# Kernel optimization log

Measured on AMD Instinct MI355X. Metric: run time of the kernel, lower is better.

## Reference

```python
import jax, jax.numpy as jnp
import numpy as np

B, S, H, NH = 8, 1024, 1024, 4
D = H // NH
NEG = jnp.float32(-2**32 + 1)


def setup_inputs() -> dict:
    key = jax.random.key(0)
    ks = jax.random.split(key, 12)
    w = 1.0 / np.sqrt(H)
    wf = 1.0 / np.sqrt(2 * H)
    return {
        "memory": jax.random.normal(ks[0], (B, S, H), jnp.float32),
        "decoder_input": jax.random.normal(ks[1], (B, S, H), jnp.float32),
        "mask": jax.random.bernoulli(ks[2], 0.2, (B, S, S)),
        "query_mask": (jax.random.uniform(ks[3], (B, S)) > 0.1).astype(jnp.float32),
        "Wk": jax.random.normal(ks[4], (H, H), jnp.float32) * w,
        "Wv": jax.random.normal(ks[5], (H, H), jnp.float32) * w,
        "Wq": jax.random.normal(ks[6], (H, H), jnp.float32) * w,
        "Wf": jax.random.normal(ks[7], (2 * H, H), jnp.float32) * wf,
        "bf": jnp.zeros((H,), jnp.float32),
        "gamma": jnp.ones((H,), jnp.float32),
        "beta": jnp.zeros((H,), jnp.float32),
        "g_factor": jax.random.uniform(ks[8], (1,), jnp.float32, 1e4, 2e4),
    }


def reference(memory, decoder_input, mask, query_mask, Wk, Wv, Wq, Wf, bf, gamma, beta, g_factor):
    b, sq, hdim = decoder_input.shape
    sk = memory.shape[1]

    def heads(x, W, s):  # -> (NH, B, s, D), matching torch permute(2,0,1,3)
        return (x @ W).reshape(b, s, NH, D).transpose(2, 0, 1, 3)

    k = heads(memory, Wk, sk)
    v = heads(memory, Wv, sk)
    q = heads(decoder_input, Wq, sq)

    attn = jnp.einsum("hbqd,hbkd->hbqk", q, k) / jnp.sqrt(jnp.float32(D))
    idx = jnp.arange(sk, dtype=jnp.float32)
    gauss = (idx[:, None] - idx[None, :]) ** 2 / g_factor[0]  # (sq, sk), sq==sk
    attn = attn - gauss
    attn = jnp.where(mask[None], NEG, attn)
    attn = jax.nn.softmax(attn, axis=-1)
    attn = attn * query_mask[None, :, :, None]  # post-softmax query mask

    res = jnp.einsum("hbqk,hbkd->hbqd", attn, v)
    res = res.transpose(1, 2, 0, 3).reshape(b, sq, hdim)

    out = jnp.concatenate([decoder_input, res], axis=-1) @ Wf + bf
    out = out + decoder_input
    mu = out.mean(-1, keepdims=True)
    var = ((out - mu) ** 2).mean(-1, keepdims=True)
    out = (out - mu) / jnp.sqrt(var + 1e-5) * gamma + beta
    return out, attn.reshape(NH * b, sq, sk)
```

## Files before the change

kernel.cpp:

```cpp
#include <hip/hip_runtime.h>

#define B_ 8
#define S_ 1024
#define H_ 1024
#define NH_ 4
#define D_ 256
#define M_ 8192

typedef unsigned int u32;
typedef unsigned short u16;
typedef __attribute__((ext_vector_type(4))) float f32x4;
typedef __attribute__((ext_vector_type(8))) short s16x8;

__device__ __forceinline__ float bf2f(u16 b) { return __uint_as_float(((u32)b) << 16); }
__device__ __forceinline__ u16 f2bf(float f) {
    u32 x = __float_as_uint(f);
    return (u16)((x + 0x7fffu + ((x >> 16) & 1u)) >> 16);
}

__global__ void init_flags_k(int* fl) { fl[0] = 0; fl[1] = 0; fl[2] = 0; }

__global__ __launch_bounds__(256) void or_mask_k(const u32* __restrict__ m, int* __restrict__ fl) {
    u32 v = m[blockIdx.x * 256 + threadIdx.x];
#pragma unroll
    for (int o = 32; o; o >>= 1) v |= __shfl_xor(v, o, 64);
    if ((threadIdx.x & 63) == 0) atomicOr(fl + 1, (int)v);
}

__global__ void classify_mask_k(int* fl) {
    u32 R = (u32)fl[1];
    int c;
    if (R == 0x3F803F80u)      c = 2;
    else if (R == 0x3F800000u) c = 3;
    else if (R & 0xFFFFFF00u)  c = 0;
    else                       c = 1;
    fl[2] = c;
}

__global__ __launch_bounds__(256) void tcast_k(const float* __restrict__ src, u16* __restrict__ dst,
                                               int R, int C) {
    __shared__ float sb[32][33];
    const int c0 = blockIdx.x * 32, r0 = blockIdx.y * 32;
    const int tx = threadIdx.x & 31, ty = threadIdx.x >> 5;
#pragma unroll
    for (int i = 0; i < 4; i++)
        sb[ty + 8 * i][tx] = src[(size_t)(r0 + ty + 8 * i) * C + c0 + tx];
    __syncthreads();
#pragma unroll
    for (int i = 0; i < 4; i++)
        dst[(size_t)(c0 + ty + 8 * i) * R + r0 + tx] = f2bf(sb[tx][ty + 8 * i]);
}

template<int AMODE>
__device__ __forceinline__ void gemm_core(
    const float* __restrict__ A32, const u16* __restrict__ A16, int lda,
    const u16* __restrict__ Bp, int ldb, int K, int m0, int n0,
    short* As, short* Bs, f32x4 acc[4][4])
{
    const int t = threadIdx.x;
    const int lane = t & 63, wave = t >> 6;
    const int wy = wave >> 1, wx = wave & 1;
    const int mq = lane >> 4, ml = lane & 15;
    const int srow = t >> 2, skq = t & 3;

    for (int k0 = 0; k0 < K; k0 += 32) {
        __syncthreads();
#pragma unroll
        for (int it = 0; it < 2; it++) {
            const int row = srow + it * 64;
            const int kk = k0 + skq * 8;
            short* dst = As + row * 40 + skq * 8;
            if (AMODE == 0) {
                const float* s = A32 + (size_t)(m0 + row) * lda + kk;
                float4 v0 = *(const float4*)s, v1 = *(const float4*)(s + 4);
                s16x8 p;
                p[0] = (short)f2bf(v0.x); p[1] = (short)f2bf(v0.y);
                p[2] = (short)f2bf(v0.z); p[3] = (short)f2bf(v0.w);
                p[4] = (short)f2bf(v1.x); p[5] = (short)f2bf(v1.y);
                p[6] = (short)f2bf(v1.z); p[7] = (short)f2bf(v1.w);
                *(s16x8*)dst = p;
            } else if (AMODE == 1) {
                *(s16x8*)dst = *(const s16x8*)(A16 + (size_t)(m0 + row) * lda + kk);
            } else {
                if (kk < 1024) {
                    const float* s = A32 + (size_t)(m0 + row) * 1024 + kk;
                    float4 v0 = *(const float4*)s, v1 = *(const float4*)(s + 4);
                    s16x8 p;
                    p[0] = (short)f2bf(v0.x); p[1] = (short)f2bf(v0.y);
                    p[2] = (short)f2bf(v0.z); p[3] = (short)f2bf(v0.w);
                    p[4] = (short)f2bf(v1.x); p[5] = (short)f2bf(v1.y);
                    p[6] = (short)f2bf(v1.z); p[7] = (short)f2bf(v1.w);
                    *(s16x8*)dst = p;
                } else {
                    *(s16x8*)dst = *(const s16x8*)(A16 + (size_t)(m0 + row) * 1024 + (kk - 1024));
                }
            }
        }
#pragma unroll
        for (int it = 0; it < 2; it++) {
            const int row = srow + it * 64;
            *(s16x8*)(Bs + row * 40 + skq * 8) =
                *(const s16x8*)(Bp + (size_t)(n0 + row) * ldb + k0 + skq * 8);
        }
        __syncthreads();
        s16x8 af[4], bfr[4];
#pragma unroll
        for (int i = 0; i < 4; i++) {
            af[i]  = *(s16x8*)(As + (wy * 64 + i * 16 + ml) * 40 + mq * 8);
            bfr[i] = *(s16x8*)(Bs + (wx * 64 + i * 16 + ml) * 40 + mq * 8);
        }
#pragma unroll
        for (int mi = 0; mi < 4; mi++)
#pragma unroll
            for (int ni = 0; ni < 4; ni++)
                acc[mi][ni] = __builtin_amdgcn_mfma_f32_16x16x32_bf16(af[mi], bfr[ni], acc[mi][ni], 0, 0, 0);
    }
}

__global__ __launch_bounds__(256) void gemm_proj_k(const float* __restrict__ A, const u16* __restrict__ WT,
                                                   u16* __restrict__ C) {
    __shared__ short As[128 * 40];
    __shared__ short Bs[128 * 40];
    const int m0 = blockIdx.y * 128, n0 = blockIdx.x * 128;
    f32x4 acc[4][4];
#pragma unroll
    for (int i = 0; i < 4; i++)
#pragma unroll
        for (int j = 0; j < 4; j++) acc[i][j] = 0;
    gemm_core<0>(A, nullptr, H_, WT, H_, H_, m0, n0, As, Bs, acc);
    const int lane = threadIdx.x & 63, wave = threadIdx.x >> 6;
    const int wy = wave >> 1, wx = wave & 1, mq = lane >> 4, ml = lane & 15;
#pragma unroll
    for (int mi = 0; mi < 4; mi++)
#pragma unroll
        for (int ni = 0; ni < 4; ni++) {
            const int n = n0 + wx * 64 + ni * 16 + ml;
#pragma unroll
            for (int r = 0; r < 4; r++) {
                const int m = m0 + wy * 64 + mi * 16 + mq * 4 + r;
                C[(size_t)m * H_ + n] = f2bf(acc[mi][ni][r]);
            }
        }
}

__global__ __launch_bounds__(256) void gemm_vt_k(const float* __restrict__ A, const u16* __restrict__ WT,
                                                 u16* __restrict__ VT) {
    __shared__ short As[128 * 40];
    __shared__ short Bs[128 * 40];
    const int m0 = blockIdx.y * 128, n0 = blockIdx.x * 128;
    f32x4 acc[4][4];
#pragma unroll
    for (int i = 0; i < 4; i++)
#pragma unroll
        for (int j = 0; j < 4; j++) acc[i][j] = 0;
    gemm_core<0>(A, nullptr, H_, WT, H_, H_, m0, n0, As, Bs, acc);
    const int lane = threadIdx.x & 63, wave = threadIdx.x >> 6;
    const int wy = wave >> 1, wx = wave & 1, mq = lane >> 4, ml = lane & 15;
#pragma unroll
    for (int mi = 0; mi < 4; mi++)
#pragma unroll
        for (int ni = 0; ni < 4; ni++) {
            const int n = n0 + wx * 64 + ni * 16 + ml;
            const int mbase = m0 + wy * 64 + mi * 16 + mq * 4;
            const int b = mbase >> 10, s = mbase & 1023;
            ushort4 w;
            w.x = f2bf(acc[mi][ni][0]); w.y = f2bf(acc[mi][ni][1]);
            w.z = f2bf(acc[mi][ni][2]); w.w = f2bf(acc[mi][ni][3]);
            *(ushort4*)(VT + ((size_t)(b * 1024 + n)) * 1024 + s) = w;
        }
}

__global__ __launch_bounds__(256) void qk_logits_k(const u16* __restrict__ Qb, const u16* __restrict__ Kb,
                                                   const void* __restrict__ mask,
                                                   const float* __restrict__ gfac, const int* __restrict__ fl,
                                                   float* __restrict__ logits) {
    __shared__ short As[128 * 40];
    __shared__ short Bs[128 * 40];
    const int z = blockIdx.z, h = z >> 3, b = z & 7;
    const u16* Aq = Qb + (size_t)b * S_ * H_ + h * D_;
    const u16* Bk = Kb + (size_t)b * S_ * H_ + h * D_;
    const int m0 = blockIdx.y * 128, n0 = blockIdx.x * 128;
    f32x4 acc[4][4];
#pragma unroll
    for (int i = 0; i < 4; i++)
#pragma unroll
        for (int j = 0; j < 4; j++) acc[i][j] = 0;
    gemm_core<1>(nullptr, Aq, H_, Bk, H_, D_, m0, n0, As, Bs, acc);
    const float g = gfac[0];
    const int code = fl[2];
    const int lane = threadIdx.x & 63, wave = threadIdx.x >> 6;
    const int wy = wave >> 1, wx = wave & 1, mq = lane >> 4, ml = lane & 15;
#pragma unroll
    for (int mi = 0; mi < 4; mi++)
#pragma unroll
        for (int ni = 0; ni < 4; ni++) {
            const int kg = n0 + wx * 64 + ni * 16 + ml;
#pragma unroll
            for (int r = 0; r < 4; r++) {
                const int qg = m0 + wy * 64 + mi * 16 + mq * 4 + r;
                float diff = (float)(qg - kg);
                float val = acc[mi][ni][r] * 0.0625f - diff * diff / g;
                size_t midx = ((size_t)b * S_ + qg) * S_ + kg;
                int mv;
                if (code == 0)      mv = ((const unsigned char*)mask)[midx];
                else if (code == 1) mv = ((const int*)mask)[midx];
                else if (code == 2) mv = (((const u16*)mask)[midx] != 0);
                else                mv = (((const u32*)mask)[midx] != 0);
                if (mv) val = -4294967296.0f;
                logits[((size_t)z * S_ + qg) * S_ + kg] = val;
            }
        }
}

__global__ __launch_bounds__(256) void softmax_k(float* __restrict__ logits, const float* __restrict__ qmask) {
    const int row = blockIdx.x;
    const int b = (row >> 10) & 7, qg = row & 1023;
    float* p = logits + (size_t)row * S_;
    const int t = threadIdx.x, wave = t >> 6;
    float4 v = ((const float4*)p)[t];
    __shared__ float red[4];
    float mx = fmaxf(fmaxf(v.x, v.y), fmaxf(v.z, v.w));
#pragma unroll
    for (int o = 32; o; o >>= 1) mx = fmaxf(mx, __shfl_xor(mx, o, 64));
    if ((t & 63) == 0) red[wave] = mx;
    __syncthreads();
    mx = fmaxf(fmaxf(red[0], red[1]), fmaxf(red[2], red[3]));
    __syncthreads();
    v.x = __expf(v.x - mx); v.y = __expf(v.y - mx);
    v.z = __expf(v.z - mx); v.w = __expf(v.w - mx);
    float s = v.x + v.y + v.z + v.w;
#pragma unroll
    for (int o = 32; o; o >>= 1) s += __shfl_xor(s, o, 64);
    if ((t & 63) == 0) red[wave] = s;
    __syncthreads();
    s = red[0] + red[1] + red[2] + red[3];
    const float sc = qmask[b * S_ + qg] / s;
    v.x *= sc; v.y *= sc; v.z *= sc; v.w *= sc;
    ((float4*)p)[t] = v;
}

__global__ __launch_bounds__(256) void pv_mfma_k(const float* __restrict__ attnF, const u16* __restrict__ VT,
                                                 u16* __restrict__ resB) {
    __shared__ short As[128 * 40];
    __shared__ short Bs[128 * 40];
    const int z = blockIdx.z, h = z >> 3, b = z & 7;
    const float* Ap = attnF + (size_t)z * S_ * S_;
    const u16* Bp = VT + ((size_t)(b * 1024 + h * D_)) * 1024;
    const int m0 = blockIdx.y * 128, n0 = blockIdx.x * 128;
    f32x4 acc[4][4];
#pragma unroll
    for (int i = 0; i < 4; i++)
#pragma unroll
        for (int j = 0; j < 4; j++) acc[i][j] = 0;
    gemm_core<0>(Ap, nullptr, S_, Bp, 1024, S_, m0, n0, As, Bs, acc);
    u16* C = resB + (size_t)b * S_ * H_ + h * D_;
    const int lane = threadIdx.x & 63, wave = threadIdx.x >> 6;
    const int wy = wave >> 1, wx = wave & 1, mq = lane >> 4, ml = lane & 15;
#pragma unroll
    for (int mi = 0; mi < 4; mi++)
#pragma unroll
        for (int ni = 0; ni < 4; ni++) {
            const int n = n0 + wx * 64 + ni * 16 + ml;
#pragma unroll
            for (int r = 0; r < 4; r++) {
                const int m = m0 + wy * 64 + mi * 16 + mq * 4 + r;
                C[(size_t)m * H_ + n] = f2bf(acc[mi][ni][r]);
            }
        }
}

__global__ __launch_bounds__(256) void final_mfma_k(const float* __restrict__ dec, const u16* __restrict__ resB,
                                                    const u16* __restrict__ WfT, const float* __restrict__ bfv,
                                                    u16* __restrict__ tmp) {
    __shared__ short As[128 * 40];
    __shared__ short Bs[128 * 40];
    const int m0 = blockIdx.y * 128, n0 = blockIdx.x * 128;
    f32x4 acc[4][4];
#pragma unroll
    for (int i = 0; i < 4; i++)
#pragma unroll
        for (int j = 0; j < 4; j++) acc[i][j] = 0;
    gemm_core<2>(dec, resB, H_, WfT, 2048, 2048, m0, n0, As, Bs, acc);
    const int lane = threadIdx.x & 63, wave = threadIdx.x >> 6;
    const int wy = wave >> 1, wx = wave & 1, mq = lane >> 4, ml = lane & 15;
#pragma unroll
    for (int mi = 0; mi < 4; mi++)
#pragma unroll
        for (int ni = 0; ni < 4; ni++) {
            const int n = n0 + wx * 64 + ni * 16 + ml;
#pragma unroll
            for (int r = 0; r < 4; r++) {
                const int m = m0 + wy * 64 + mi * 16 + mq * 4 + r;
                float val = acc[mi][ni][r] + bfv[n] + dec[(size_t)m * H_ + n];
                tmp[(size_t)m * H_ + n] = f2bf(val);
            }
        }
}

__global__ __launch_bounds__(256) void ln2_k(const u16* __restrict__ tmp, const float* __restrict__ gm,
                                             const float* __restrict__ bt, float* __restrict__ out) {
    const int m = blockIdx.x, t = threadIdx.x;
    ushort4 u = ((const ushort4*)(tmp + (size_t)m * H_))[t];
    float xa[4] = {bf2f(u.x), bf2f(u.y), bf2f(u.z), bf2f(u.w)};
    float s = 0.f, s2 = 0.f;
#pragma unroll
    for (int i = 0; i < 4; i++) { s += xa[i]; s2 += xa[i] * xa[i]; }
#pragma unroll
    for (int o = 32; o; o >>= 1) { s += __shfl_xor(s, o, 64); s2 += __shfl_xor(s2, o, 64); }
    __shared__ float rs[4], rs2[4];
    if ((t & 63) == 0) { rs[t >> 6] = s; rs2[t >> 6] = s2; }
    __syncthreads();
    s  = rs[0] + rs[1] + rs[2] + rs[3];
    s2 = rs2[0] + rs2[1] + rs2[2] + rs2[3];
    float mu = s * (1.f / 1024.f);
    float var = s2 * (1.f / 1024.f) - mu * mu;
    float rstd = rsqrtf(var + 1e-5f);
    float ov[4];
#pragma unroll
    for (int i = 0; i < 4; i++) {
        int n = t * 4 + i;
        ov[i] = (xa[i] - mu) * rstd * gm[n] + bt[n];
    }
    *(float4*)(out + (size_t)m * H_ + t * 4) = make_float4(ov[0], ov[1], ov[2], ov[3]);
}

extern "C" void kernel_launch(void* const* d_in, const int* in_sizes, int n_in,
                              void* d_out, int out_size, void* d_ws, size_t ws_size,
                              hipStream_t stream) {
    const float* memory = (const float*)d_in[0];
    const float* dec    = (const float*)d_in[1];
    const void*  mask   = d_in[2];
    const float* qmask  = (const float*)d_in[3];
    const float* Wk     = (const float*)d_in[4];
    const float* Wv     = (const float*)d_in[5];
    const float* Wq     = (const float*)d_in[6];
    const float* Wf     = (const float*)d_in[7];
    const float* bfv    = (const float*)d_in[8];
    const float* gamma  = (const float*)d_in[9];
    const float* beta   = (const float*)d_in[10];
    const float* gfac   = (const float*)d_in[11];

    char* ws = (char*)d_ws;
    int* fl  = (int*)ws;
    u16* WqT = (u16*)(ws + (1u  << 20));
    u16* WkT = (u16*)(ws + (3u  << 20));
    u16* WvT = (u16*)(ws + (5u  << 20));
    u16* WfT = (u16*)(ws + (7u  << 20));
    u16* Qb  = (u16*)(ws + (11u << 20));
    u16* Kb  = (u16*)(ws + (27u << 20));
    u16* VT  = (u16*)(ws + (43u << 20));
    u16* resB = Kb;
    u16* tmpB = Qb;

    float* out   = (float*)d_out;
    float* attnF = out + (size_t)B_ * S_ * H_;

    init_flags_k<<<1, 1, 0, stream>>>(fl);
    or_mask_k<<<256, 256, 0, stream>>>((const u32*)mask, fl);
    classify_mask_k<<<1, 1, 0, stream>>>(fl);

    tcast_k<<<dim3(32, 32), 256, 0, stream>>>(Wq, WqT, 1024, 1024);
    tcast_k<<<dim3(32, 32), 256, 0, stream>>>(Wk, WkT, 1024, 1024);
    tcast_k<<<dim3(32, 32), 256, 0, stream>>>(Wv, WvT, 1024, 1024);
    tcast_k<<<dim3(32, 64), 256, 0, stream>>>(Wf, WfT, 2048, 1024);

    gemm_proj_k<<<dim3(8, 64), 256, 0, stream>>>(dec,    WqT, Qb);
    gemm_proj_k<<<dim3(8, 64), 256, 0, stream>>>(memory, WkT, Kb);
    gemm_vt_k  <<<dim3(8, 64), 256, 0, stream>>>(memory, WvT, VT);

    qk_logits_k<<<dim3(8, 8, 32), 256, 0, stream>>>(Qb, Kb, mask, gfac, fl, attnF);
    softmax_k<<<32768, 256, 0, stream>>>(attnF, qmask);
    pv_mfma_k<<<dim3(2, 8, 32), 256, 0, stream>>>(attnF, VT, resB);
    final_mfma_k<<<dim3(8, 64), 256, 0, stream>>>(dec, resB, WfT, bfv, tmpB);
    ln2_k<<<M_, 256, 0, stream>>>(tmpB, gamma, beta, out);
}
```

Measured before the change: 696.1 us.

## Fuse QK logits with row softmax and pre-cast projection inputs to bf16

```diff
diff --git a/kernel.cpp b/kernel.cpp
--- a/kernel.cpp
+++ b/kernel.cpp
@@ -49,6 +49,14 @@
 #pragma unroll
     for (int i = 0; i < 4; i++)
         dst[(size_t)(c0 + ty + 8 * i) * R + r0 + tx] = f2bf(sb[tx][ty + 8 * i]);
+}
+
+__global__ __launch_bounds__(256) void castbf_k(const float* __restrict__ src, u16* __restrict__ dst) {
+    const int i = blockIdx.x * 256 + threadIdx.x;
+    float4 v = ((const float4*)src)[i];
+    ushort4 o;
+    o.x = f2bf(v.x); o.y = f2bf(v.y); o.z = f2bf(v.z); o.w = f2bf(v.w);
+    ((ushort4*)dst)[i] = o;
 }
 
 template<int AMODE>
@@ -117,7 +125,7 @@
     }
 }
 
-__global__ __launch_bounds__(256) void gemm_proj_k(const float* __restrict__ A, const u16* __restrict__ WT,
+__global__ __launch_bounds__(256) void gemm_proj_k(const u16* __restrict__ A, const u16* __restrict__ WT,
                                                    u16* __restrict__ C) {
     __shared__ short As[128 * 40];
     __shared__ short Bs[128 * 40];
@@ -127,7 +135,7 @@
     for (int i = 0; i < 4; i++)
 #pragma unroll
         for (int j = 0; j < 4; j++) acc[i][j] = 0;
-    gemm_core<0>(A, nullptr, H_, WT, H_, H_, m0, n0, As, Bs, acc);
+    gemm_core<1>(nullptr, A, H_, WT, H_, H_, m0, n0, As, Bs, acc);
     const int lane = threadIdx.x & 63, wave = threadIdx.x >> 6;
     const int wy = wave >> 1, wx = wave & 1, mq = lane >> 4, ml = lane & 15;
 #pragma unroll
@@ -143,7 +151,7 @@
         }
 }
 
-__global__ __launch_bounds__(256) void gemm_vt_k(const float* __restrict__ A, const u16* __restrict__ WT,
+__global__ __launch_bounds__(256) void gemm_vt_k(const u16* __restrict__ A, const u16* __restrict__ WT,
                                                  u16* __restrict__ VT) {
     __shared__ short As[128 * 40];
     __shared__ short Bs[128 * 40];
@@ -153,7 +161,7 @@
     for (int i = 0; i < 4; i++)
 #pragma unroll
         for (int j = 0; j < 4; j++) acc[i][j] = 0;
-    gemm_core<0>(A, nullptr, H_, WT, H_, H_, m0, n0, As, Bs, acc);
+    gemm_core<1>(nullptr, A, H_, WT, H_, H_, m0, n0, As, Bs, acc);
     const int lane = threadIdx.x & 63, wave = threadIdx.x >> 6;
     const int wy = wave >> 1, wx = wave & 1, mq = lane >> 4, ml = lane & 15;
 #pragma unroll
@@ -170,73 +178,161 @@
         }
 }
 
-__global__ __launch_bounds__(256) void qk_logits_k(const u16* __restrict__ Qb, const u16* __restrict__ Kb,
-                                                   const void* __restrict__ mask,
-                                                   const float* __restrict__ gfac, const int* __restrict__ fl,
-                                                   float* __restrict__ logits) {
-    __shared__ short As[128 * 40];
-    __shared__ short Bs[128 * 40];
-    const int z = blockIdx.z, h = z >> 3, b = z & 7;
+__global__ __launch_bounds__(512, 2) void qk_sm_k(
+    const u16* __restrict__ Qb, const u16* __restrict__ Kb,
+    const void* __restrict__ mask, const float* __restrict__ gfac,
+    const int* __restrict__ fl, const float* __restrict__ qmask,
+    float* __restrict__ attn)
+{
+    __shared__ short Bs[1024 * 40];
+    __shared__ short As[64 * 40];
+    __shared__ float red[2][32][4];
+
+    const int flat = blockIdx.x;
+    const int wgid = (flat & 7) * 64 + (flat >> 3);
+    const int z = wgid >> 4, m0 = (wgid & 15) * 64;
+    const int h = z >> 3, b = z & 7;
+
     const u16* Aq = Qb + (size_t)b * S_ * H_ + h * D_;
     const u16* Bk = Kb + (size_t)b * S_ * H_ + h * D_;
-    const int m0 = blockIdx.y * 128, n0 = blockIdx.x * 128;
-    f32x4 acc[4][4];
-#pragma unroll
-    for (int i = 0; i < 4; i++)
-#pragma unroll
-        for (int j = 0; j < 4; j++) acc[i][j] = 0;
-    gemm_core<1>(nullptr, Aq, H_, Bk, H_, D_, m0, n0, As, Bs, acc);
-    const float g = gfac[0];
+
+    const int t = threadIdx.x;
+    const int lane = t & 63, wave = t >> 6;
+    const int wm = wave >> 2, wn = wave & 3;
+    const int mq = lane >> 4, ml = lane & 15;
+
+    f32x4 acc[2][16];
+#pragma unroll
+    for (int mi = 0; mi < 2; mi++)
+#pragma unroll
+        for (int nf = 0; nf < 16; nf++) acc[mi][nf] = 0;
+
+    for (int k0 = 0; k0 < D_; k0 += 32) {
+        __syncthreads();
+        if (t < 256) {
+            const int row = t >> 2, kq = t & 3;
+            *(s16x8*)(As + row * 40 + kq * 8) =
+                *(const s16x8*)(Aq + (size_t)(m0 + row) * H_ + k0 + kq * 8);
+        }
+#pragma unroll
+        for (int it = 0; it < 8; it++) {
+            const int c = it * 512 + t;
+            const int row = c >> 2, kq = c & 3;
+            *(s16x8*)(Bs + row * 40 + kq * 8) =
+                *(const s16x8*)(Bk + (size_t)row * H_ + k0 + kq * 8);
+        }
+        __syncthreads();
+        s16x8 af0 = *(s16x8*)(As + (wm * 32 + ml) * 40 + mq * 8);
+        s16x8 af1 = *(s16x8*)(As + (wm * 32 + 16 + ml) * 40 + mq * 8);
+#pragma unroll
+        for (int g4 = 0; g4 < 4; g4++) {
+            s16x8 bf4[4];
+#pragma unroll
+            for (int j = 0; j < 4; j++)
+                bf4[j] = *(s16x8*)(Bs + (wn * 256 + (g4 * 4 + j) * 16 + ml) * 40 + mq * 8);
+#pragma unroll
+            for (int j = 0; j < 4; j++) {
+                acc[0][g4 * 4 + j] = __builtin_amdgcn_mfma_f32_16x16x32_bf16(af0, bf4[j], acc[0][g4 * 4 + j], 0, 0, 0);
+                acc[1][g4 * 4 + j] = __builtin_amdgcn_mfma_f32_16x16x32_bf16(af1, bf4[j], acc[1][g4 * 4 + j], 0, 0, 0);
+            }
+        }
+    }
+
+    const float ginv = 1.0f / gfac[0];
     const int code = fl[2];
-    const int lane = threadIdx.x & 63, wave = threadIdx.x >> 6;
-    const int wy = wave >> 1, wx = wave & 1, mq = lane >> 4, ml = lane & 15;
-#pragma unroll
-    for (int mi = 0; mi < 4; mi++)
-#pragma unroll
-        for (int ni = 0; ni < 4; ni++) {
-            const int kg = n0 + wx * 64 + ni * 16 + ml;
-#pragma unroll
-            for (int r = 0; r < 4; r++) {
-                const int qg = m0 + wy * 64 + mi * 16 + mq * 4 + r;
+    const size_t zrow = (size_t)z * S_;
+    float rmax[2][4], rsum[2][4], scv[2][4];
+
+#pragma unroll
+    for (int mi = 0; mi < 2; mi++)
+#pragma unroll
+        for (int r = 0; r < 4; r++) {
+            const int qg = m0 + wm * 32 + mi * 16 + mq * 4 + r;
+            const size_t mbase = ((size_t)b * S_ + qg) * S_;
+            float mx = -3.0e38f;
+#pragma unroll
+            for (int nf = 0; nf < 16; nf++) {
+                const int kg = wn * 256 + nf * 16 + ml;
                 float diff = (float)(qg - kg);
-                float val = acc[mi][ni][r] * 0.0625f - diff * diff / g;
-                size_t midx = ((size_t)b * S_ + qg) * S_ + kg;
+                float val = acc[mi][nf][r] * 0.0625f - diff * diff * ginv;
                 int mv;
-                if (code == 0)      mv = ((const unsigned char*)mask)[midx];
-                else if (code == 1) mv = ((const int*)mask)[midx];
-                else if (code == 2) mv = (((const u16*)mask)[midx] != 0);
-                else                mv = (((const u32*)mask)[midx] != 0);
+                if (code == 0)      mv = ((const unsigned char*)mask)[mbase + kg];
+                else if (code == 1) mv = ((const int*)mask)[mbase + kg];
+                else if (code == 2) mv = (((const u16*)mask)[mbase + kg] != 0);
+                else                mv = (((const u32*)mask)[mbase + kg] != 0);
                 if (mv) val = -4294967296.0f;
-                logits[((size_t)z * S_ + qg) * S_ + kg] = val;
-            }
-        }
-}
-
-__global__ __launch_bounds__(256) void softmax_k(float* __restrict__ logits, const float* __restrict__ qmask) {
-    const int row = blockIdx.x;
-    const int b = (row >> 10) & 7, qg = row & 1023;
-    float* p = logits + (size_t)row * S_;
-    const int t = threadIdx.x, wave = t >> 6;
-    float4 v = ((const float4*)p)[t];
-    __shared__ float red[4];
-    float mx = fmaxf(fmaxf(v.x, v.y), fmaxf(v.z, v.w));
-#pragma unroll
-    for (int o = 32; o; o >>= 1) mx = fmaxf(mx, __shfl_xor(mx, o, 64));
-    if ((t & 63) == 0) red[wave] = mx;
+                acc[mi][nf][r] = val;
+                mx = fmaxf(mx, val);
+            }
+            rmax[mi][r] = mx;
+        }
+#pragma unroll
+    for (int o = 1; o < 16; o <<= 1)
+#pragma unroll
+        for (int mi = 0; mi < 2; mi++)
+#pragma unroll
+            for (int r = 0; r < 4; r++)
+                rmax[mi][r] = fmaxf(rmax[mi][r], __shfl_xor(rmax[mi][r], o, 64));
+    if (ml == 0)
+#pragma unroll
+        for (int mi = 0; mi < 2; mi++)
+#pragma unroll
+            for (int r = 0; r < 4; r++) red[wm][mi * 16 + mq * 4 + r][wn] = rmax[mi][r];
     __syncthreads();
-    mx = fmaxf(fmaxf(red[0], red[1]), fmaxf(red[2], red[3]));
+#pragma unroll
+    for (int mi = 0; mi < 2; mi++)
+#pragma unroll
+        for (int r = 0; r < 4; r++) {
+            const int rr = mi * 16 + mq * 4 + r;
+            rmax[mi][r] = fmaxf(fmaxf(red[wm][rr][0], red[wm][rr][1]),
+                                fmaxf(red[wm][rr][2], red[wm][rr][3]));
+        }
     __syncthreads();
-    v.x = __expf(v.x - mx); v.y = __expf(v.y - mx);
-    v.z = __expf(v.z - mx); v.w = __expf(v.w - mx);
-    float s = v.x + v.y + v.z + v.w;
-#pragma unroll
-    for (int o = 32; o; o >>= 1) s += __shfl_xor(s, o, 64);
-    if ((t & 63) == 0) red[wave] = s;
+#pragma unroll
+    for (int mi = 0; mi < 2; mi++)
+#pragma unroll
+        for (int r = 0; r < 4; r++) {
+            float s = 0.f;
+#pragma unroll
+            for (int nf = 0; nf < 16; nf++) {
+                float p = __expf(acc[mi][nf][r] - rmax[mi][r]);
+                acc[mi][nf][r] = p;
+                s += p;
+            }
+            rsum[mi][r] = s;
+        }
+#pragma unroll
+    for (int o = 1; o < 16; o <<= 1)
+#pragma unroll
+        for (int mi = 0; mi < 2; mi++)
+#pragma unroll
+            for (int r = 0; r < 4; r++) rsum[mi][r] += __shfl_xor(rsum[mi][r], o, 64);
+    if (ml == 0)
+#pragma unroll
+        for (int mi = 0; mi < 2; mi++)
+#pragma unroll
+            for (int r = 0; r < 4; r++) red[wm][mi * 16 + mq * 4 + r][wn] = rsum[mi][r];
     __syncthreads();
-    s = red[0] + red[1] + red[2] + red[3];
-    const float sc = qmask[b * S_ + qg] / s;
-    v.x *= sc; v.y *= sc; v.z *= sc; v.w *= sc;
-    ((float4*)p)[t] = v;
+#pragma unroll
+    for (int mi = 0; mi < 2; mi++)
+#pragma unroll
+        for (int r = 0; r < 4; r++) {
+            const int rr = mi * 16 + mq * 4 + r;
+            const int qg = m0 + wm * 32 + mi * 16 + mq * 4 + r;
+            const float s = red[wm][rr][0] + red[wm][rr][1] + red[wm][rr][2] + red[wm][rr][3];
+            scv[mi][r] = qmask[b * S_ + qg] / s;
+        }
+#pragma unroll
+    for (int mi = 0; mi < 2; mi++)
+#pragma unroll
+        for (int r = 0; r < 4; r++) {
+            const int qg = m0 + wm * 32 + mi * 16 + mq * 4 + r;
+            float* prow = attn + (zrow + qg) * S_ + wn * 256 + ml;
+            const float sc = scv[mi][r];
+#pragma unroll
+            for (int nf = 0; nf < 16; nf++)
+                prow[nf * 16] = acc[mi][nf][r] * sc;
+        }
 }
 
 __global__ __launch_bounds__(256) void pv_mfma_k(const float* __restrict__ attnF, const u16* __restrict__ VT,
@@ -355,6 +451,9 @@
     float* out   = (float*)d_out;
     float* attnF = out + (size_t)B_ * S_ * H_;
 
+    u16* memB = (u16*)attnF;
+    u16* decB = memB + (size_t)B_ * S_ * H_;
+
     init_flags_k<<<1, 1, 0, stream>>>(fl);
     or_mask_k<<<256, 256, 0, stream>>>((const u32*)mask, fl);
     classify_mask_k<<<1, 1, 0, stream>>>(fl);
@@ -364,12 +463,14 @@
     tcast_k<<<dim3(32, 32), 256, 0, stream>>>(Wv, WvT, 1024, 1024);
     tcast_k<<<dim3(32, 64), 256, 0, stream>>>(Wf, WfT, 2048, 1024);
 
-    gemm_proj_k<<<dim3(8, 64), 256, 0, stream>>>(dec,    WqT, Qb);
-    gemm_proj_k<<<dim3(8, 64), 256, 0, stream>>>(memory, WkT, Kb);
-    gemm_vt_k  <<<dim3(8, 64), 256, 0, stream>>>(memory, WvT, VT);
-
-    qk_logits_k<<<dim3(8, 8, 32), 256, 0, stream>>>(Qb, Kb, mask, gfac, fl, attnF);
-    softmax_k<<<32768, 256, 0, stream>>>(attnF, qmask);
+    castbf_k<<<8192, 256, 0, stream>>>(memory, memB);
+    castbf_k<<<8192, 256, 0, stream>>>(dec,    decB);
+
+    gemm_proj_k<<<dim3(8, 64), 256, 0, stream>>>(decB, WqT, Qb);
+    gemm_proj_k<<<dim3(8, 64), 256, 0, stream>>>(memB, WkT, Kb);
+    gemm_vt_k  <<<dim3(8, 64), 256, 0, stream>>>(memB, WvT, VT);
+
+    qk_sm_k<<<512, 512, 0, stream>>>(Qb, Kb, mask, gfac, fl, qmask, attnF);
     pv_mfma_k<<<dim3(2, 8, 32), 256, 0, stream>>>(attnF, VT, resB);
     final_mfma_k<<<dim3(8, 64), 256, 0, stream>>>(dec, resB, WfT, bfv, tmpB);
     ln2_k<<<M_, 256, 0, stream>>>(tmpB, gamma, beta, out);
```

After: 634.2 us. 8.9% less time.
